# Performance work log

Measured on AMD Instinct MI355X. Metric: run time of the kernel, lower is better.

The kernel has to match this reference:

```python
import jax, jax.numpy as jnp
import numpy as np

B, T, C, H = 2, 2048, 1024, 16
D = C // H  # head dim = 64

def setup_inputs() -> dict:
    key = jax.random.key(0)
    ks = jax.random.split(key, 5)
    s = 1.0 / np.sqrt(C)
    return {
        "x": jax.random.normal(ks[0], (B, T, C), jnp.float32),
        "Wq": jax.random.normal(ks[1], (C, C), jnp.float32) * s,
        "Wk": jax.random.normal(ks[2], (C, C), jnp.float32) * s,
        "Wv": jax.random.normal(ks[3], (C, C), jnp.float32) * s,
        "Wo": jax.random.normal(ks[4], (C, C), jnp.float32) * s,
    }

def reference(x, Wq, Wk, Wv, Wo):
    # torch Linear: y = x @ W.T  (weights stored [out, in])
    def proj(W):
        h = jnp.einsum('btc,oc->bto', x, W)
        return h.reshape(B, T, H, D).transpose(0, 2, 1, 3)  # [B,H,T,D]
    q, k, v = proj(Wq), proj(Wk), proj(Wv)
    scale = 1.0 / np.sqrt(D)
    att = jnp.einsum('bhqd,bhkd->bhqk', q, k) * scale  # [B,H,T,T]
    causal = jnp.tril(jnp.ones((T, T), bool))
    att = jnp.where(causal[None, None], att, -jnp.inf)
    att = jax.nn.softmax(att, axis=-1)
    y = jnp.einsum('bhqk,bhkd->bhqd', att, v)  # [B,H,T,D]
    y = y.transpose(0, 2, 1, 3).reshape(B, T, C)
    return jnp.einsum('btc,oc->bto', y, Wo)
```

## Files before the change

### kernel.cpp

```cpp
#include <hip/hip_runtime.h>
#include <math.h>

typedef short bf16x8 __attribute__((ext_vector_type(8)));
typedef float f32x4 __attribute__((ext_vector_type(4)));
typedef float f32x16 __attribute__((ext_vector_type(16)));
typedef int int2v __attribute__((ext_vector_type(2)));

constexpr int Bc = 2, Tc = 2048, Cc = 1024, Hc = 16, Dc = 64;
constexpr int Mc = Bc * Tc;

#if __has_builtin(__builtin_amdgcn_exp2f)
#define EXP2(x) __builtin_amdgcn_exp2f(x)
#else
#define EXP2(x) exp2f(x)
#endif

#define SBAR() do { asm volatile("" ::: "memory"); \
                    __builtin_amdgcn_s_barrier();   \
                    asm volatile("" ::: "memory"); } while (0)

__device__ __forceinline__ unsigned short f2bf(float f) {
    union { float f; unsigned u; } v; v.f = f;
    unsigned r = v.u + 0x7fffu + ((v.u >> 16) & 1u);
    return (unsigned short)(r >> 16);
}

__device__ __forceinline__ float bf2f(unsigned short u) {
    union { unsigned u; float f; } v; v.u = (unsigned)u << 16; return v.f;
}

__device__ __forceinline__ unsigned cvt_pk_bf16(float lo, float hi) {
    unsigned r;
    asm("v_cvt_pk_bf16_f32 %0, %1, %2" : "=v"(r) : "v"(lo), "v"(hi));
    return r;
}

__device__ __forceinline__ void gload16(const void* g, void* l) {
    __builtin_amdgcn_global_load_lds(
        (const __attribute__((address_space(1))) void*)g,
        (__attribute__((address_space(3))) void*)l, 16, 0, 0);
}

__global__ __launch_bounds__(256)
void cast_bf16(const float* __restrict__ in, unsigned short* __restrict__ out, int n8) {
    int i = blockIdx.x * 256 + threadIdx.x;
    if (i >= n8) return;
    const float4* p = (const float4*)in;
    float4 a = p[i * 2], b = p[i * 2 + 1];
    union { unsigned short u[8]; bf16x8 v; } r;
    r.u[0] = f2bf(a.x); r.u[1] = f2bf(a.y); r.u[2] = f2bf(a.z); r.u[3] = f2bf(a.w);
    r.u[4] = f2bf(b.x); r.u[5] = f2bf(b.y); r.u[6] = f2bf(b.z); r.u[7] = f2bf(b.w);
    *(bf16x8*)(out + i * 8) = r.v;
}

__global__ __launch_bounds__(256)
void cast_w4(const float* __restrict__ a, const float* __restrict__ b,
             const float* __restrict__ c, const float* __restrict__ d,
             unsigned short* __restrict__ oa, unsigned short* __restrict__ ob,
             unsigned short* __restrict__ oc, unsigned short* __restrict__ od) {
    const float* src = blockIdx.y == 0 ? a : blockIdx.y == 1 ? b : blockIdx.y == 2 ? c : d;
    unsigned short* dst = blockIdx.y == 0 ? oa : blockIdx.y == 1 ? ob : blockIdx.y == 2 ? oc : od;
    int i = blockIdx.x * 256 + threadIdx.x;
    const float4* p = (const float4*)src;
    float4 x = p[i * 2], y = p[i * 2 + 1];
    union { unsigned short u[8]; bf16x8 v; } r;
    r.u[0] = f2bf(x.x); r.u[1] = f2bf(x.y); r.u[2] = f2bf(x.z); r.u[3] = f2bf(x.w);
    r.u[4] = f2bf(y.x); r.u[5] = f2bf(y.y); r.u[6] = f2bf(y.z); r.u[7] = f2bf(y.w);
    *(bf16x8*)(dst + i * 8) = r.v;
}

__global__ __launch_bounds__(256)
void gemm_qkv(const unsigned short* __restrict__ A,
              const unsigned short* __restrict__ Wq,
              const unsigned short* __restrict__ Wk,
              const unsigned short* __restrict__ Wv,
              unsigned short* __restrict__ Qo,
              unsigned short* __restrict__ Ko,
              unsigned short* __restrict__ Vo) {
    __shared__ unsigned short As[128 * 32];
    __shared__ unsigned short Bs[128 * 32];
    const int t = threadIdx.x;
    const int lane = t & 63, l15 = lane & 15, l4 = lane >> 4;
    const int w = t >> 6, wr = w >> 1, wc = w & 1;
    const int seg = blockIdx.y >> 3;
    const unsigned short* W = seg == 0 ? Wq : seg == 1 ? Wk : Wv;
    const int m0 = blockIdx.x * 128, n0 = (blockIdx.y & 7) * 128;

    f32x4 acc[4][4] = {};

    for (int k0 = 0; k0 < Cc; k0 += 32) {
        __syncthreads();
        #pragma unroll
        for (int it = 0; it < 2; ++it) {
            int c = t + it * 256;
            int row = c >> 2, ko = (c & 3) << 3;
            gload16(A + (size_t)(m0 + row) * Cc + k0 + ko, As + c * 8);
            gload16(W + (size_t)(n0 + row) * Cc + k0 + ko, Bs + c * 8);
        }
        __syncthreads();
        bf16x8 af[4], bfr[4];
        #pragma unroll
        for (int i = 0; i < 4; ++i)
            af[i] = *(const bf16x8*)(As + ((wr * 64 + i * 16 + l15) * 32 + l4 * 8));
        #pragma unroll
        for (int j = 0; j < 4; ++j)
            bfr[j] = *(const bf16x8*)(Bs + ((wc * 64 + j * 16 + l15) * 32 + l4 * 8));
        #pragma unroll
        for (int i = 0; i < 4; ++i)
            #pragma unroll
            for (int j = 0; j < 4; ++j)
                acc[i][j] = __builtin_amdgcn_mfma_f32_16x16x32_bf16(af[i], bfr[j], acc[i][j], 0, 0, 0);
    }

    const float qscale = 0.18033688011112042f;
    const int r0 = wr * 64 + (l4 << 2);
    const int c0 = wc * 64 + l15;
    #pragma unroll
    for (int i = 0; i < 4; ++i)
        #pragma unroll
        for (int j = 0; j < 4; ++j)
            #pragma unroll
            for (int r = 0; r < 4; ++r) {
                int row = m0 + r0 + i * 16 + r;
                int col = n0 + c0 + j * 16;
                float v = acc[i][j][r];
                int bb = row >> 11, tt = row & (Tc - 1);
                int hh = col >> 6, dd = col & 63;
                if (seg == 0)
                    Qo[((((size_t)bb * Hc + hh) * Tc + tt) << 6) + dd] = f2bf(v * qscale);
                else if (seg == 1)
                    Ko[((((size_t)bb * Hc + hh) * Tc + tt) << 6) + dd] = f2bf(v);
                else
                    Vo[(((size_t)bb * Hc + hh) * Dc + dd) * Tc + tt] = f2bf(v);
            }
}

__global__ __launch_bounds__(256)
void gemm_out(const unsigned short* __restrict__ A,
              const unsigned short* __restrict__ W,
              float* __restrict__ outp) {
    __shared__ unsigned short As[64 * 32];
    __shared__ unsigned short Bs[64 * 32];
    const int t = threadIdx.x;
    const int lane = t & 63, l15 = lane & 15, l4 = lane >> 4;
    const int w = t >> 6, wr = w >> 1, wc = w & 1;
    const int m0 = blockIdx.x * 64, n0 = blockIdx.y * 64;

    f32x4 acc[2][2] = {};

    for (int k0 = 0; k0 < Cc; k0 += 32) {
        __syncthreads();
        {
            int row = t >> 2, ko = (t & 3) << 3;
            gload16(A + (size_t)(m0 + row) * Cc + k0 + ko, As + t * 8);
            gload16(W + (size_t)(n0 + row) * Cc + k0 + ko, Bs + t * 8);
        }
        __syncthreads();
        bf16x8 af[2], bfr[2];
        #pragma unroll
        for (int i = 0; i < 2; ++i)
            af[i] = *(const bf16x8*)(As + ((wr * 32 + i * 16 + l15) * 32 + l4 * 8));
        #pragma unroll
        for (int j = 0; j < 2; ++j)
            bfr[j] = *(const bf16x8*)(Bs + ((wc * 32 + j * 16 + l15) * 32 + l4 * 8));
        #pragma unroll
        for (int i = 0; i < 2; ++i)
            #pragma unroll
            for (int j = 0; j < 2; ++j)
                acc[i][j] = __builtin_amdgcn_mfma_f32_16x16x32_bf16(af[i], bfr[j], acc[i][j], 0, 0, 0);
    }

    const int r0 = wr * 32 + (l4 << 2);
    const int c0 = wc * 32 + l15;
    #pragma unroll
    for (int i = 0; i < 2; ++i)
        #pragma unroll
        for (int j = 0; j < 2; ++j)
            #pragma unroll
            for (int r = 0; r < 4; ++r)
                outp[(size_t)(m0 + r0 + i * 16 + r) * Cc + n0 + c0 + j * 16] = acc[i][j][r];
}

__device__ __constant__ unsigned char JOBS[34] = {
    61, 62,
    60, 56, 57, 58, 54, 36, 37,
    52, 53, 49, 50, 32, 33,
    48, 44, 45, 46, 42, 28, 29, 12,
    40, 41, 24, 25,
    20, 21, 8,
    16, 17,
    4, 0
};

__global__ __launch_bounds__(256)
void attn_mfma(const unsigned short* __restrict__ Q,
               const unsigned short* __restrict__ K,
               const unsigned short* __restrict__ Vt,
               unsigned short* __restrict__ Y,
               unsigned short* __restrict__ P1,
               unsigned short* __restrict__ P2,
               float* __restrict__ mlf) {
    __shared__ unsigned short Ks[2][64 * 64];
    __shared__ unsigned short Vs[2][64 * 64];

    const int t = threadIdx.x, lane = t & 63, w = t >> 6;
    const int l31 = lane & 31, h = lane >> 5;
    const int bh = blockIdx.x;
    const int bb = bh >> 4, hh = bh & 15;

    const unsigned char job = JOBS[blockIdx.y];
    const int c = job >> 2, p = job & 3;
    const int n = 2 * c + 2;
    const int npart = c < 4 ? 1 : (c < 10 ? 2 : 3);
    const int kb0 = p * n / npart;
    const int kb1 = (p + 1) * n / npart;

    const int qbase = c * 128 + w * 32;
    const int q = qbase + l31;

    const unsigned short* Qp = Q + (size_t)bh * Tc * Dc;
    const unsigned short* Kp = K + (size_t)bh * Tc * Dc;
    const unsigned short* Vp = Vt + (size_t)bh * Dc * Tc;

    bf16x8 qf[4];
    #pragma unroll
    for (int kc = 0; kc < 4; ++kc)
        qf[kc] = *(const bf16x8*)(Qp + (size_t)q * 64 + kc * 16 + h * 8);

    f32x16 ot[2] = {};
    float m = -INFINITY, lsum = 0.f;

    auto stage = [&](int kb, int buf) {
        #pragma unroll
        for (int it = 0; it < 2; ++it) {
            int idx = t + it * 256;
            int row = idx >> 3, slot = idx & 7;
            int ss = slot ^ (row & 7);
            gload16(Kp + (size_t)(kb * 64 + row) * 64 + ss * 8, &Ks[buf][idx * 8]);
            gload16(Vp + (size_t)row * Tc + kb * 64 + ss * 8, &Vs[buf][idx * 8]);
        }
    };

    stage(kb0, 0);
    if (kb0 + 1 < kb1) stage(kb0 + 1, 1);

    for (int kb = kb0; kb < kb1; ++kb) {
        const int cur = (kb - kb0) & 1;
        if (kb + 1 < kb1) asm volatile("s_waitcnt vmcnt(4)" ::: "memory");
        else              asm volatile("s_waitcnt vmcnt(0)" ::: "memory");
        SBAR();

        const bool active = (kb * 64 <= qbase + 31);
        if (active) {
            f32x16 st[2] = {};
            __builtin_amdgcn_s_setprio(1);
            #pragma unroll
            for (int nt = 0; nt < 2; ++nt) {
                int key = nt * 32 + l31;
                #pragma unroll
                for (int kc = 0; kc < 4; ++kc) {
                    int boff = (kc * 32 + h * 16) ^ ((key & 7) << 4);
                    bf16x8 kf = *(const bf16x8*)(&Ks[cur][((key << 7) + boff) >> 1]);
                    st[nt] = __builtin_amdgcn_mfma_f32_32x32x16_bf16(kf, qf[kc], st[nt], 0, 0, 0);
                }
            }
            __builtin_amdgcn_s_setprio(0);

            if (kb * 64 + 63 > qbase) {
                #pragma unroll
                for (int nt = 0; nt < 2; ++nt)
                    #pragma unroll
                    for (int r = 0; r < 16; ++r) {
                        int key = kb * 64 + nt * 32 + (r & 3) + 8 * (r >> 2) + 4 * h;
                        if (key > q) st[nt][r] = -1e30f;
                    }
            }

            float mx[16];
            #pragma unroll
            for (int r = 0; r < 16; ++r) mx[r] = fmaxf(st[0][r], st[1][r]);
            #pragma unroll
            for (int s2 = 8; s2 > 0; s2 >>= 1)
                #pragma unroll
                for (int r = 0; r < s2; ++r) mx[r] = fmaxf(mx[r], mx[r + s2]);
            float tmax = fmaxf(mx[0], __shfl_xor(mx[0], 32));

            if (__any(tmax > m + 8.f)) {
                float mn = fmaxf(m, tmax);
                float al = EXP2(m - mn);
                m = mn;
                lsum *= al;
                #pragma unroll
                for (int dt = 0; dt < 2; ++dt)
                    #pragma unroll
                    for (int r = 0; r < 16; ++r) ot[dt][r] *= al;
            }

            float psa[4] = {0.f, 0.f, 0.f, 0.f};
            #pragma unroll
            for (int nt = 0; nt < 2; ++nt)
                #pragma unroll
                for (int r = 0; r < 16; ++r) {
                    float pv = EXP2(st[nt][r] - m);
                    st[nt][r] = pv;
                    psa[r & 3] += pv;
                }
            lsum += (psa[0] + psa[1]) + (psa[2] + psa[3]);

            #pragma unroll
            for (int nt = 0; nt < 2; ++nt) {
                unsigned a0 = cvt_pk_bf16(st[nt][0],  st[nt][1]);
                unsigned b0 = cvt_pk_bf16(st[nt][4],  st[nt][5]);
                unsigned a1 = cvt_pk_bf16(st[nt][2],  st[nt][3]);
                unsigned b1 = cvt_pk_bf16(st[nt][6],  st[nt][7]);
                int2v r0 = __builtin_amdgcn_permlane32_swap((int)a0, (int)b0, false, false);
                int2v r1 = __builtin_amdgcn_permlane32_swap((int)a1, (int)b1, false, false);
                union { unsigned u[4]; bf16x8 v; } pf0, pf1;
                pf0.u[0] = r0.x; pf0.u[1] = r1.x; pf0.u[2] = r0.y; pf0.u[3] = r1.y;
                unsigned c0 = cvt_pk_bf16(st[nt][8],  st[nt][9]);
                unsigned d0 = cvt_pk_bf16(st[nt][12], st[nt][13]);
                unsigned c1 = cvt_pk_bf16(st[nt][10], st[nt][11]);
                unsigned d1 = cvt_pk_bf16(st[nt][14], st[nt][15]);
                int2v r2 = __builtin_amdgcn_permlane32_swap((int)c0, (int)d0, false, false);
                int2v r3 = __builtin_amdgcn_permlane32_swap((int)c1, (int)d1, false, false);
                pf1.u[0] = r2.x; pf1.u[1] = r3.x; pf1.u[2] = r2.y; pf1.u[3] = r3.y;

                __builtin_amdgcn_s_setprio(1);
                #pragma unroll
                for (int dt = 0; dt < 2; ++dt) {
                    int d = dt * 32 + l31;
                    int v0off = (nt * 64 + h * 16) ^ ((d & 7) << 4);
                    bf16x8 vf0 = *(const bf16x8*)(&Vs[cur][((d << 7) + v0off) >> 1]);
                    ot[dt] = __builtin_amdgcn_mfma_f32_32x32x16_bf16(vf0, pf0.v, ot[dt], 0, 0, 0);
                }
                #pragma unroll
                for (int dt = 0; dt < 2; ++dt) {
                    int d = dt * 32 + l31;
                    int v1off = (nt * 64 + 32 + h * 16) ^ ((d & 7) << 4);
                    bf16x8 vf1 = *(const bf16x8*)(&Vs[cur][((d << 7) + v1off) >> 1]);
                    ot[dt] = __builtin_amdgcn_mfma_f32_32x32x16_bf16(vf1, pf1.v, ot[dt], 0, 0, 0);
                }
                __builtin_amdgcn_s_setprio(0);
            }
        }

        SBAR();
        if (kb + 2 < kb1) stage(kb + 2, cur);
    }

    float lf = lsum + __shfl_xor(lsum, 32);
    unsigned short* dst;
    size_t base;
    if (npart == 1 || p == 0) {
        dst = Y;  base = ((size_t)bb * Tc + q) * Cc + hh * 64;
    } else if (p == 1) {
        dst = P1; base = ((size_t)(bb * 1536 + (q - 512))) * Cc + hh * 64;
    } else {
        dst = P2; base = ((size_t)(bb * 768 + (q - 1280))) * Cc + hh * 64;
    }
    float inv = (npart == 1) ? 1.f / lf : 1.f;
    #pragma unroll
    for (int dt = 0; dt < 2; ++dt)
        #pragma unroll
        for (int rg = 0; rg < 4; ++rg) {
            int d0 = dt * 32 + rg * 8 + 4 * h;
            ushort4 s4;
            s4.x = f2bf(ot[dt][rg * 4 + 0] * inv);
            s4.y = f2bf(ot[dt][rg * 4 + 1] * inv);
            s4.z = f2bf(ot[dt][rg * 4 + 2] * inv);
            s4.w = f2bf(ot[dt][rg * 4 + 3] * inv);
            *(ushort4*)(dst + base + d0) = s4;
        }
    if (npart > 1 && h == 0) {
        int mi = p * 49152 + bh * 1536 + (q - 512);
        mlf[mi]          = m;
        mlf[147456 + mi] = lf;
    }
}

__global__ __launch_bounds__(256)
void attn_combine(unsigned short* __restrict__ Y,
                  const unsigned short* __restrict__ P1,
                  const unsigned short* __restrict__ P2,
                  const float* __restrict__ mlf) {
    int tid = blockIdx.x * 256 + threadIdx.x;
    int rowIdx = tid >> 7;
    int col8 = (tid & 127) * 8;
    int bb = rowIdx / 1536, qoff = rowIdx % 1536;
    int q = 512 + qoff;
    int hh = col8 >> 6;
    int mi = (bb * 16 + hh) * 1536 + qoff;
    bool three = q >= 1280;

    float m0 = mlf[mi],          l0 = mlf[147456 + mi];
    float m1 = mlf[49152 + mi],  l1 = mlf[196608 + mi];
    float m2 = three ? mlf[98304 + mi]  : -INFINITY;
    float l2 = three ? mlf[245760 + mi] : 0.f;

    float M = fmaxf(fmaxf(m0, m1), m2);
    float a0 = exp2f(m0 - M), a1 = exp2f(m1 - M);
    float a2 = three ? exp2f(m2 - M) : 0.f;
    float inv = 1.f / (l0 * a0 + l1 * a1 + l2 * a2);

    size_t offY = ((size_t)(bb * Tc + q)) * Cc + col8;
    size_t off1 = ((size_t)rowIdx) * Cc + col8;
    union { unsigned short u[8]; bf16x8 v; } y0, y1, y2, r;
    y0.v = *(const bf16x8*)(Y + offY);
    y1.v = *(const bf16x8*)(P1 + off1);
    if (three) {
        size_t off2 = ((size_t)(bb * 768 + (q - 1280))) * Cc + col8;
        y2.v = *(const bf16x8*)(P2 + off2);
    }
    #pragma unroll
    for (int j = 0; j < 8; ++j) {
        float acc = bf2f(y0.u[j]) * a0 + bf2f(y1.u[j]) * a1;
        if (three) acc += bf2f(y2.u[j]) * a2;
        r.u[j] = f2bf(acc * inv);
    }
    *(bf16x8*)(Y + offY) = r.v;
}

extern "C" void kernel_launch(void* const* d_in, const int* in_sizes, int n_in,
                              void* d_out, int out_size, void* d_ws, size_t ws_size,
                              hipStream_t stream) {
    const float* x  = (const float*)d_in[0];
    const float* Wq = (const float*)d_in[1];
    const float* Wk = (const float*)d_in[2];
    const float* Wv = (const float*)d_in[3];
    const float* Wo = (const float*)d_in[4];

    unsigned short* ws = (unsigned short*)d_ws;
    const size_t nX = (size_t)Mc * Cc;
    const size_t nW = (size_t)Cc * Cc;
    size_t off = 0;
    unsigned short* xb  = ws + off; off += nX;
    unsigned short* Wqb = ws + off; off += nW;
    unsigned short* Wkb = ws + off; off += nW;
    unsigned short* Wvb = ws + off; off += nW;
    unsigned short* Wob = ws + off; off += nW;
    unsigned short* Qw  = ws + off; off += nX;
    unsigned short* Kw  = ws + off; off += nX;
    unsigned short* Vtw = ws + off; off += nX;
    unsigned short* Yb  = ws + off; off += nX;

    dim3 blk(256);
    cast_bf16<<<dim3((int)(nX / 8 / 256)), blk, 0, stream>>>(x, xb, (int)(nX / 8));
    cast_w4<<<dim3(512, 4), blk, 0, stream>>>(Wq, Wk, Wv, Wo, Wqb, Wkb, Wvb, Wob);

    gemm_qkv<<<dim3(Mc / 128, 24), blk, 0, stream>>>(xb, Wqb, Wkb, Wvb, Qw, Kw, Vtw);

    unsigned short* P1 = xb;
    unsigned short* P2 = Wqb;
    float* mlf = (float*)Wvb;
    attn_mfma<<<dim3(Bc * Hc, 34), blk, 0, stream>>>(Qw, Kw, Vtw, Yb, P1, P2, mlf);
    attn_combine<<<dim3(1536), blk, 0, stream>>>(Yb, P1, P2, mlf);

    gemm_out<<<dim3(Mc / 64, Cc / 64), blk, 0, stream>>>(Yb, Wob, (float*)d_out);
}
```

Before: 114.4 us.

## Double-buffer QKV GEMM with 256x256 tiles, 512 threads and swizzled LDS

Reworks the QKV projection GEMM to use 256x256 block tiles with 8 waves, double-buffered LDS, and global loads for tile k+2 issued while tile k is computed, using explicit vmcnt waits. It XOR-swizzles the LDS chunk layout to reduce bank conflicts and raises wave priority around the MFMA loop. The goal is to hide global-load latency and increase operand reuse per tile. The trade-off is a grid of only 192 blocks, which may underfill the GPU, plus higher register and LDS pressure from 32 accumulators per wave.

Result: slower. 139.4 us (+21.9%).

```diff
diff --git a/kernel.cpp b/kernel.cpp
--- a/kernel.cpp
+++ b/kernel.cpp
@@ -69,7 +69,7 @@
     *(bf16x8*)(dst + i * 8) = r.v;
 }
 
-__global__ __launch_bounds__(256)
+__global__ __launch_bounds__(512)
 void gemm_qkv(const unsigned short* __restrict__ A,
               const unsigned short* __restrict__ Wq,
               const unsigned short* __restrict__ Wk,
@@ -77,53 +77,75 @@
               unsigned short* __restrict__ Qo,
               unsigned short* __restrict__ Ko,
               unsigned short* __restrict__ Vo) {
-    __shared__ unsigned short As[128 * 32];
-    __shared__ unsigned short Bs[128 * 32];
+    __shared__ unsigned short As[2][256 * 32];
+    __shared__ unsigned short Bs[2][256 * 32];
     const int t = threadIdx.x;
     const int lane = t & 63, l15 = lane & 15, l4 = lane >> 4;
-    const int w = t >> 6, wr = w >> 1, wc = w & 1;
-    const int seg = blockIdx.y >> 3;
+    const int w = t >> 6;
+    const int wm = w >> 2, wn = w & 3;
+    const int seg = blockIdx.y >> 2;
     const unsigned short* W = seg == 0 ? Wq : seg == 1 ? Wk : Wv;
-    const int m0 = blockIdx.x * 128, n0 = (blockIdx.y & 7) * 128;
-
-    f32x4 acc[4][4] = {};
-
-    for (int k0 = 0; k0 < Cc; k0 += 32) {
-        __syncthreads();
+    const int m0 = blockIdx.x * 256, n0 = (blockIdx.y & 3) * 256;
+
+    f32x4 acc[8][4] = {};
+
+    auto stageKT = [&](int kt) {
+        const int s = kt & 1;
         #pragma unroll
         for (int it = 0; it < 2; ++it) {
-            int c = t + it * 256;
-            int row = c >> 2, ko = (c & 3) << 3;
-            gload16(A + (size_t)(m0 + row) * Cc + k0 + ko, As + c * 8);
-            gload16(W + (size_t)(n0 + row) * Cc + k0 + ko, Bs + c * 8);
-        }
-        __syncthreads();
-        bf16x8 af[4], bfr[4];
-        #pragma unroll
-        for (int i = 0; i < 4; ++i)
-            af[i] = *(const bf16x8*)(As + ((wr * 64 + i * 16 + l15) * 32 + l4 * 8));
-        #pragma unroll
-        for (int j = 0; j < 4; ++j)
-            bfr[j] = *(const bf16x8*)(Bs + ((wc * 64 + j * 16 + l15) * 32 + l4 * 8));
-        #pragma unroll
-        for (int i = 0; i < 4; ++i)
-            #pragma unroll
-            for (int j = 0; j < 4; ++j)
-                acc[i][j] = __builtin_amdgcn_mfma_f32_16x16x32_bf16(af[i], bfr[j], acc[i][j], 0, 0, 0);
+            int idx = t + it * 512;
+            int row = idx >> 2, sl = idx & 3;
+            int ss = sl ^ ((row >> 1) & 3);
+            gload16(A + (size_t)(m0 + row) * Cc + kt * 32 + ss * 8, &As[s][idx * 8]);
+            gload16(W + (size_t)(n0 + row) * Cc + kt * 32 + ss * 8, &Bs[s][idx * 8]);
+        }
+    };
+
+    stageKT(0);
+    stageKT(1);
+
+    const int NKT = Cc / 32;
+    for (int kt = 0; kt < NKT; ++kt) {
+        const int s = kt & 1;
+        if (kt + 1 < NKT) asm volatile("s_waitcnt vmcnt(4)" ::: "memory");
+        else              asm volatile("s_waitcnt vmcnt(0)" ::: "memory");
+        SBAR();
+
+        bf16x8 af[8], bf[4];
+        #pragma unroll
+        for (int ii = 0; ii < 8; ++ii) {
+            int row = wm * 128 + ii * 16 + l15;
+            int ch = l4 ^ ((row >> 1) & 3);
+            af[ii] = *(const bf16x8*)(&As[s][row * 32 + ch * 8]);
+        }
+        #pragma unroll
+        for (int jj = 0; jj < 4; ++jj) {
+            int row = wn * 64 + jj * 16 + l15;
+            int ch = l4 ^ ((row >> 1) & 3);
+            bf[jj] = *(const bf16x8*)(&Bs[s][row * 32 + ch * 8]);
+        }
+        __builtin_amdgcn_s_setprio(1);
+        #pragma unroll
+        for (int ii = 0; ii < 8; ++ii)
+            #pragma unroll
+            for (int jj = 0; jj < 4; ++jj)
+                acc[ii][jj] = __builtin_amdgcn_mfma_f32_16x16x32_bf16(af[ii], bf[jj], acc[ii][jj], 0, 0, 0);
+        __builtin_amdgcn_s_setprio(0);
+
+        SBAR();
+        if (kt + 2 < NKT) stageKT(kt + 2);
     }
 
     const float qscale = 0.18033688011112042f;
-    const int r0 = wr * 64 + (l4 << 2);
-    const int c0 = wc * 64 + l15;
     #pragma unroll
-    for (int i = 0; i < 4; ++i)
-        #pragma unroll
-        for (int j = 0; j < 4; ++j)
+    for (int ii = 0; ii < 8; ++ii)
+        #pragma unroll
+        for (int jj = 0; jj < 4; ++jj)
             #pragma unroll
             for (int r = 0; r < 4; ++r) {
-                int row = m0 + r0 + i * 16 + r;
-                int col = n0 + c0 + j * 16;
-                float v = acc[i][j][r];
+                int row = m0 + wm * 128 + ii * 16 + (l4 << 2) + r;
+                int col = n0 + wn * 64 + jj * 16 + l15;
+                float v = acc[ii][jj][r];
                 int bb = row >> 11, tt = row & (Tc - 1);
                 int hh = col >> 6, dd = col & 63;
                 if (seg == 0)
@@ -447,7 +469,7 @@
     cast_bf16<<<dim3((int)(nX / 8 / 256)), blk, 0, stream>>>(x, xb, (int)(nX / 8));
     cast_w4<<<dim3(512, 4), blk, 0, stream>>>(Wq, Wk, Wv, Wo, Wqb, Wkb, Wvb, Wob);
 
-    gemm_qkv<<<dim3(Mc / 128, 24), blk, 0, stream>>>(xb, Wqb, Wkb, Wvb, Qw, Kw, Vtw);
+    gemm_qkv<<<dim3(Mc / 256, 12), dim3(512), 0, stream>>>(xb, Wqb, Wkb, Wvb, Qw, Kw, Vtw);
 
     unsigned short* P1 = xb;
     unsigned short* P2 = Wqb;
```
